# Kernel optimization log

Measured on AMD Instinct MI355X. Metric: run time of the kernel, lower is better.

The kernel has to match this reference:

```python
import jax, jax.numpy as jnp
import numpy as np

EPS = 1e-10

def _quantize_one(x, codebook):
    # x: [B, T, D]; codebook: [K, D]
    B, T, D = x.shape
    K = codebook.shape[0]
    flat = x.reshape(-1, D)  # [N, D]
    # squared euclidean distance (argmin of this == argmax of -dist in torch code)
    dist = (jnp.sum(flat * flat, axis=-1, keepdims=True)
            - 2.0 * flat @ codebook.T
            + jnp.sum(codebook * codebook, axis=-1))  # [N, K]
    ind = jnp.argmin(dist, axis=-1)  # [N]
    q = codebook[ind].reshape(B, T, D)
    # commitment loss: mse(quantize.detach(), x) * commitment(=1.0)
    loss = jnp.mean((jax.lax.stop_gradient(q) - x) ** 2)
    # straight-through estimator
    q_st = x + jax.lax.stop_gradient(q - x)
    # perplexity from one-hot encodings
    counts = jnp.zeros((K,), dtype=x.dtype).at[ind].add(1.0)
    avg_probs = counts / ind.shape[0]
    perplexity = jnp.exp(-jnp.sum(avg_probs * jnp.log(avg_probs + EPS)))
    return q_st, loss, perplexity

def setup_inputs() -> dict:
    key = jax.random.key(0)
    k1, k2 = jax.random.split(key)
    z = jax.random.normal(k1, (16, 64, 4096), dtype=jnp.float32)
    codebooks = jax.random.normal(k2, (8, 1024, 64), dtype=jnp.float32)
    return {"z": z, "codebooks": codebooks}

def reference(z, codebooks):
    # z: [B, code_dim, T] -> transpose(2,1) -> [B, T, code_dim]
    x = jnp.transpose(z, (0, 2, 1))

    def step(carry, cb):
        residual, quantized_out = carry
        q, loss, perp = _quantize_one(residual, cb)
        return (residual - q, quantized_out + q), (loss, perp)

    (_, quantized_out), (losses, perplexities) = jax.lax.scan(
        step, (x, jnp.zeros_like(x)), codebooks)
    zq = jnp.transpose(quantized_out, (0, 2, 1))  # back to [B, code_dim, T]
    return zq, losses, perplexities
```

## Files before the change

### kernel.cpp

```cpp
#include <hip/hip_runtime.h>

#define S      8
#define K      1024
#define D      64
#define NVEC   65536
#define NW     4096
#define NELEM  4194304.0f
#define EPSQ   1e-10f
#define DELTA  0.005f

typedef __attribute__((ext_vector_type(8))) short  short8;
typedef __attribute__((ext_vector_type(4))) float  float4v;

static __device__ inline unsigned short f2bf(float f) {
    unsigned int u = __float_as_uint(f);
    u = (u + 0x7FFFu + ((u >> 16) & 1u)) >> 16;
    return (unsigned short)u;
}
static __device__ inline float bf2f(unsigned short h) {
    return __uint_as_float(((unsigned int)h) << 16);
}

__global__ void rvq_prep(const float* __restrict__ cb,
                         unsigned short* __restrict__ cbi,
                         float* __restrict__ c2, unsigned* __restrict__ cnt) {
    int i = blockIdx.x * blockDim.x + threadIdx.x;
    if (i < S * K) {
        const float* row = cb + (size_t)i * D;
        float a0 = 0.f, a1 = 0.f, a2 = 0.f, a3 = 0.f;
#pragma unroll
        for (int d = 0; d < D; d += 4) {
            a0 = fmaf(row[d+0], row[d+0], a0);
            a1 = fmaf(row[d+1], row[d+1], a1);
            a2 = fmaf(row[d+2], row[d+2], a2);
            a3 = fmaf(row[d+3], row[d+3], a3);
        }
        c2[i] = (a0 + a1) + (a2 + a3);
        cnt[i] = 0u;
    }
    int s  = i >> 12;
    int tau = (i >> 6) & 63;
    int l  = i & 63;
    int m  = l & 15, qq = l >> 4;
    const float* row = cb + (size_t)(s * K + tau * 16 + m) * D;
    short8 h0h, h0l, h1h, h1l;
#pragma unroll
    for (int e = 0; e < 8; ++e) {
        float x = -2.0f * row[qq * 8 + e];
        unsigned short h = f2bf(x);
        h0h[e] = (short)h; h0l[e] = (short)f2bf(x - bf2f(h));
        float y = -2.0f * row[32 + qq * 8 + e];
        unsigned short g = f2bf(y);
        h1h[e] = (short)g; h1l[e] = (short)f2bf(y - bf2f(g));
    }
    unsigned short* rec = cbi + (size_t)(s * 64 + tau) * 2048 + l * 8;
    *(short8*)(rec +    0) = h0h;
    *(short8*)(rec +  512) = h1h;
    *(short8*)(rec + 1024) = h0l;
    *(short8*)(rec + 1536) = h1l;
}

__global__ __launch_bounds__(64, 2)
void rvq_main(const float* __restrict__ z, const float* __restrict__ cbf,
              const unsigned short* __restrict__ cbi,
              const float* __restrict__ c2, float* __restrict__ zq,
              float* __restrict__ lossp, unsigned* __restrict__ cnt) {
    const int lane = threadIdx.x;
    const int m    = lane & 15;
    const int q    = lane >> 4;
    const int wid  = blockIdx.x;
    const int vbase = wid * 16;
    const int b    = vbase >> 12;
    const int ta   = (vbase & 4095) + m;
    const size_t zrow = ((size_t)(b * 64)) << 12;
    const int lo16 = lane * 16;
    const int lom  = m * 4;

    float ra0[8], ra1[8];
#pragma unroll
    for (int i = 0; i < 8; ++i) {
        ra0[i] = z[zrow + ((size_t)(q*8+i)    << 12) + ta];
        ra1[i] = z[zrow + ((size_t)(32+q*8+i) << 12) + ta];
    }

#define LOADB(i) {                                                           \
        B##i##0 = *(const short8*)(tp + lo16);                               \
        B##i##1 = *(const short8*)(tp + lo16 + 1024);                        \
        B##i##2 = *(const short8*)(tp + lo16 + 2048);                        \
        B##i##3 = *(const short8*)(tp + lo16 + 3072);                        \
        cc##i   = *(const float*)(cp + lom);                                 \
        tp += 4096; cp += 64;                                                \
    }

#define COMPUTE(i, tt) {                                                     \
        float4v a0 = {cc##i, cc##i, cc##i, cc##i};                           \
        __builtin_amdgcn_s_setprio(1);                                       \
        a0 = __builtin_amdgcn_mfma_f32_16x16x32_bf16(xa0h, B##i##0, a0, 0,0,0); \
        a0 = __builtin_amdgcn_mfma_f32_16x16x32_bf16(xa0l, B##i##0, a0, 0,0,0); \
        a0 = __builtin_amdgcn_mfma_f32_16x16x32_bf16(xa0h, B##i##2, a0, 0,0,0); \
        a0 = __builtin_amdgcn_mfma_f32_16x16x32_bf16(xa1h, B##i##1, a0, 0,0,0); \
        a0 = __builtin_amdgcn_mfma_f32_16x16x32_bf16(xa1l, B##i##1, a0, 0,0,0); \
        a0 = __builtin_amdgcn_mfma_f32_16x16x32_bf16(xa1h, B##i##3, a0, 0,0,0); \
        __builtin_amdgcn_s_setprio(0);                                       \
        const int ncol = (tt) * 16 + m;                                      \
        _Pragma("unroll")                                                    \
        for (int j = 0; j < 4; ++j) {                                        \
            float sa = a0[j];                                                \
            b2a[j] = __builtin_amdgcn_fmed3f(sa, b1a[j], b2a[j]);            \
            k1a[j] = (sa < b1a[j]) ? ncol : k1a[j];                          \
            b1a[j] = fminf(sa, b1a[j]);                                      \
        }                                                                    \
    }

#pragma unroll 1
    for (int s = 0; s < S; ++s) {
        short8 xa0h, xa0l, xa1h, xa1l;
#pragma unroll
        for (int i = 0; i < 8; ++i) {
            unsigned short h;
            h = f2bf(ra0[i]); xa0h[i] = (short)h; xa0l[i] = (short)f2bf(ra0[i] - bf2f(h));
            h = f2bf(ra1[i]); xa1h[i] = (short)h; xa1l[i] = (short)f2bf(ra1[i] - bf2f(h));
        }

        float b1a[4], b2a[4];
        int   k1a[4];
#pragma unroll
        for (int j = 0; j < 4; ++j) {
            b1a[j] = 3.4e38f; b2a[j] = 3.4e38f; k1a[j] = 0;
        }

        const float* c2s = c2 + s * K;
        const char*  tp  = (const char*)(cbi + (size_t)s * 131072);
        const char*  cp  = (const char*)c2s;

        short8 B00, B01, B02, B03, B10, B11, B12, B13;
        float  cc0, cc1;

        LOADB(0) LOADB(1)

#pragma unroll 1
        for (int it = 0; it < 31; ++it) {
            const int tau = it * 2;
            COMPUTE(0, tau + 0) LOADB(0)
            COMPUTE(1, tau + 1) LOADB(1)
        }
        COMPUTE(0, 62) COMPUTE(1, 63)

#pragma unroll
        for (int off = 1; off < 16; off <<= 1) {
#pragma unroll
            for (int j = 0; j < 4; ++j) {
                float o1 = __shfl_xor(b1a[j], off); int ok = __shfl_xor(k1a[j], off);
                float o2 = __shfl_xor(b2a[j], off);
                float n2 = fminf(fminf(b2a[j], o2), fmaxf(b1a[j], o1));
                bool tk = (o1 < b1a[j]) || (o1 == b1a[j] && ok < k1a[j]);
                k1a[j] = tk ? ok : k1a[j]; b1a[j] = fminf(b1a[j], o1); b2a[j] = n2;
            }
        }

        const float* cr0 = cbf + (size_t)s * 65536;
#define RESCUE(b1X, b2X, k1X, R0, R1)                                         \
        for (int j = 0; j < 4; ++j) {                                         \
            unsigned long long mask = __ballot(b2X[j] - b1X[j] < DELTA);      \
            while (mask) {                                                    \
                int lq = (int)(__builtin_ctzll(mask)) >> 4;                   \
                mask &= ~(0xFFFFULL << (lq * 16));                            \
                int mrow = lq * 4 + j;                                        \
                float bd = 3.4e38f; int bk = 0;                               \
                for (int cc = 0; cc < 16; ++cc) {                             \
                    int n = cc * 64 + lane;                                   \
                    const float* crow = cr0 + (size_t)n * 64;                 \
                    float dot = 0.f;                                          \
                    for (int p2 = 0; p2 < 4; ++p2) {                          \
                        for (int i = 0; i < 8; ++i)                           \
                            dot = fmaf(__shfl(R0[i], mrow + 16*p2), crow[p2*8+i], dot); \
                        for (int i = 0; i < 8; ++i)                           \
                            dot = fmaf(__shfl(R1[i], mrow + 16*p2), crow[32+p2*8+i], dot); \
                    }                                                         \
                    float sc = c2s[n] - 2.f * dot;                            \
                    if (sc < bd) { bd = sc; bk = n; }                         \
                }                                                             \
                for (int off = 1; off < 64; off <<= 1) {                      \
                    float ob = __shfl_xor(bd, off); int ok = __shfl_xor(bk, off); \
                    bool tk = (ob < bd) || (ob == bd && ok < bk);             \
                    bk = tk ? ok : bk; bd = fminf(bd, ob);                    \
                }                                                             \
                if (q == lq) k1X[j] = bk;                                     \
            }                                                                 \
        }
        RESCUE(b1a, b2a, k1a, ra0, ra1)
#undef RESCUE

        int mm = m & 3, src = (m >> 2) * 16;
        int wa0 = __shfl(k1a[0], src), wa1 = __shfl(k1a[1], src);
        int wa2 = __shfl(k1a[2], src), wa3 = __shfl(k1a[3], src);
        int bka = (mm == 0) ? wa0 : (mm == 1) ? wa1 : (mm == 2) ? wa2 : wa3;

        const float* qa = cbf + (size_t)s * 65536 + (size_t)bka * 64;
#pragma unroll
        for (int i = 0; i < 8; ++i) {
            ra0[i] -= qa[q*8+i];  ra1[i] -= qa[32+q*8+i];
        }

        float ls = 0.f;
#pragma unroll
        for (int i = 0; i < 8; ++i) {
            ls = fmaf(ra0[i], ra0[i], ls); ls = fmaf(ra1[i], ra1[i], ls);
        }
#pragma unroll
        for (int off = 1; off < 64; off <<= 1) ls += __shfl_xor(ls, off);
        if (lane == 0) lossp[s * NW + wid] = ls;

        if (q == 0) atomicAdd(&cnt[s * K + bka], 1u);
    }
#undef LOADB
#undef COMPUTE

#pragma unroll
    for (int i = 0; i < 8; ++i) {
        size_t a0 = zrow + ((size_t)(q*8+i)    << 12) + ta;
        size_t a1 = zrow + ((size_t)(32+q*8+i) << 12) + ta;
        zq[a0] = z[a0] - ra0[i];
        zq[a1] = z[a1] - ra1[i];
    }
}

__global__ void rvq_finalize(const float* __restrict__ lossp,
                             const unsigned* __restrict__ cnt,
                             float* __restrict__ out_loss,
                             float* __restrict__ out_perp) {
    const int s   = blockIdx.x;
    const int tid = threadIdx.x;
    float ent = 0.f, lsum = 0.f;
    for (int i = tid; i < K; i += 256) {
        float p = (float)cnt[s * K + i] * (1.0f / 65536.0f);
        ent += p * logf(p + EPSQ);
    }
    for (int i = tid; i < NW; i += 256) lsum += lossp[s * NW + i];
    __shared__ float redE[4], redL[4];
#pragma unroll
    for (int off = 32; off > 0; off >>= 1) {
        ent  += __shfl_down(ent, off);
        lsum += __shfl_down(lsum, off);
    }
    if ((tid & 63) == 0) { redE[tid >> 6] = ent; redL[tid >> 6] = lsum; }
    __syncthreads();
    if (tid == 0) {
        float te = redE[0] + redE[1] + redE[2] + redE[3];
        float tl = redL[0] + redL[1] + redL[2] + redL[3];
        out_perp[s] = expf(-te);
        out_loss[s] = tl * (1.0f / NELEM);
    }
}

extern "C" void kernel_launch(void* const* d_in, const int* in_sizes, int n_in,
                              void* d_out, int out_size, void* d_ws, size_t ws_size,
                              hipStream_t stream) {
    const float* z  = (const float*)d_in[0];
    const float* cb = (const float*)d_in[1];

    float* zq       = (float*)d_out;
    float* out_loss = zq + 4194304;
    float* out_perp = out_loss + 8;

    char* ws = (char*)d_ws;
    unsigned short* cbi = (unsigned short*)(ws);
    float*    c2    = (float*)(ws + 2097152);
    unsigned* cnt   = (unsigned*)(ws + 2129920);
    float*    lossp = (float*)(ws + 2162688);

    hipLaunchKernelGGL(rvq_prep,     dim3(128),  dim3(256), 0, stream, cb, cbi, c2, cnt);
    hipLaunchKernelGGL(rvq_main,     dim3(NW),   dim3(64),  0, stream, z, cb, cbi, c2, zq, lossp, cnt);
    hipLaunchKernelGGL(rvq_finalize, dim3(S),    dim3(256), 0, stream, lossp, cnt, out_loss, out_perp);
}
```

Before: 429.1 us.

## Process 32 vectors per wave sharing codebook tiles, residuals kept in LDS

Each wave now handles two 16-vector tiles, so every codebook B-fragment loaded from memory feeds two sets of MFMAs and codebook traffic per vector is halved. The MFMA chain is split into two independent accumulators per tile to shorten dependency chains and expose more instruction-level parallelism. Residuals move from registers into a padded shared-memory array, which adds LDS traffic and lowers register pressure. The grid is halved (NW 2048), which reduces the number of waves available to hide latency.

```diff
diff --git a/kernel.cpp b/kernel.cpp
--- a/kernel.cpp
+++ b/kernel.cpp
@@ -4,7 +4,7 @@
 #define K      1024
 #define D      64
 #define NVEC   65536
-#define NW     4096
+#define NW     2048
 #define NELEM  4194304.0f
 #define EPSQ   1e-10f
 #define DELTA  0.005f
@@ -69,18 +69,22 @@
     const int m    = lane & 15;
     const int q    = lane >> 4;
     const int wid  = blockIdx.x;
-    const int vbase = wid * 16;
+    const int vbase = wid * 32;
     const int b    = vbase >> 12;
     const int ta   = (vbase & 4095) + m;
+    const int tb   = ta + 16;
     const size_t zrow = ((size_t)(b * 64)) << 12;
     const int lo16 = lane * 16;
     const int lom  = m * 4;
 
-    float ra0[8], ra1[8];
+    __shared__ float rsp[32][65];
+
 #pragma unroll
     for (int i = 0; i < 8; ++i) {
-        ra0[i] = z[zrow + ((size_t)(q*8+i)    << 12) + ta];
-        ra1[i] = z[zrow + ((size_t)(32+q*8+i) << 12) + ta];
+        rsp[m][q*8+i]         = z[zrow + ((size_t)(q*8+i)    << 12) + ta];
+        rsp[m][32+q*8+i]      = z[zrow + ((size_t)(32+q*8+i) << 12) + ta];
+        rsp[16+m][q*8+i]      = z[zrow + ((size_t)(q*8+i)    << 12) + tb];
+        rsp[16+m][32+q*8+i]   = z[zrow + ((size_t)(32+q*8+i) << 12) + tb];
     }
 
 #define LOADB(i) {                                                           \
@@ -92,41 +96,53 @@
         tp += 4096; cp += 64;                                                \
     }
 
+#define MF(A,B,C) __builtin_amdgcn_mfma_f32_16x16x32_bf16(A,B,C,0,0,0)
+
 #define COMPUTE(i, tt) {                                                     \
-        float4v a0 = {cc##i, cc##i, cc##i, cc##i};                           \
+        float4v p0 = {cc##i, cc##i, cc##i, cc##i};                           \
+        float4v p1 = {0.f, 0.f, 0.f, 0.f};                                   \
+        float4v r0 = {cc##i, cc##i, cc##i, cc##i};                           \
+        float4v r1 = {0.f, 0.f, 0.f, 0.f};                                   \
         __builtin_amdgcn_s_setprio(1);                                       \
-        a0 = __builtin_amdgcn_mfma_f32_16x16x32_bf16(xa0h, B##i##0, a0, 0,0,0); \
-        a0 = __builtin_amdgcn_mfma_f32_16x16x32_bf16(xa0l, B##i##0, a0, 0,0,0); \
-        a0 = __builtin_amdgcn_mfma_f32_16x16x32_bf16(xa0h, B##i##2, a0, 0,0,0); \
-        a0 = __builtin_amdgcn_mfma_f32_16x16x32_bf16(xa1h, B##i##1, a0, 0,0,0); \
-        a0 = __builtin_amdgcn_mfma_f32_16x16x32_bf16(xa1l, B##i##1, a0, 0,0,0); \
-        a0 = __builtin_amdgcn_mfma_f32_16x16x32_bf16(xa1h, B##i##3, a0, 0,0,0); \
+        p0 = MF(xa0h, B##i##0, p0); r0 = MF(xb0h, B##i##0, r0);              \
+        p1 = MF(xa1h, B##i##1, p1); r1 = MF(xb1h, B##i##1, r1);              \
+        p0 = MF(xa0l, B##i##0, p0); r0 = MF(xb0l, B##i##0, r0);              \
+        p1 = MF(xa1l, B##i##1, p1); r1 = MF(xb1l, B##i##1, r1);              \
+        p0 = MF(xa0h, B##i##2, p0); r0 = MF(xb0h, B##i##2, r0);              \
+        p1 = MF(xa1h, B##i##3, p1); r1 = MF(xb1h, B##i##3, r1);              \
         __builtin_amdgcn_s_setprio(0);                                       \
         const int ncol = (tt) * 16 + m;                                      \
         _Pragma("unroll")                                                    \
         for (int j = 0; j < 4; ++j) {                                        \
-            float sa = a0[j];                                                \
+            float sa = p0[j] + p1[j];                                        \
             b2a[j] = __builtin_amdgcn_fmed3f(sa, b1a[j], b2a[j]);            \
             k1a[j] = (sa < b1a[j]) ? ncol : k1a[j];                          \
             b1a[j] = fminf(sa, b1a[j]);                                      \
+            float sb = r0[j] + r1[j];                                        \
+            b2b[j] = __builtin_amdgcn_fmed3f(sb, b1b[j], b2b[j]);            \
+            k1b[j] = (sb < b1b[j]) ? ncol : k1b[j];                          \
+            b1b[j] = fminf(sb, b1b[j]);                                      \
         }                                                                    \
     }
 
 #pragma unroll 1
     for (int s = 0; s < S; ++s) {
-        short8 xa0h, xa0l, xa1h, xa1l;
+        short8 xa0h, xa0l, xa1h, xa1l, xb0h, xb0l, xb1h, xb1l;
 #pragma unroll
         for (int i = 0; i < 8; ++i) {
-            unsigned short h;
-            h = f2bf(ra0[i]); xa0h[i] = (short)h; xa0l[i] = (short)f2bf(ra0[i] - bf2f(h));
-            h = f2bf(ra1[i]); xa1h[i] = (short)h; xa1l[i] = (short)f2bf(ra1[i] - bf2f(h));
-        }
-
-        float b1a[4], b2a[4];
-        int   k1a[4];
+            unsigned short h; float v;
+            v = rsp[m][q*8+i];        h = f2bf(v); xa0h[i] = (short)h; xa0l[i] = (short)f2bf(v - bf2f(h));
+            v = rsp[m][32+q*8+i];     h = f2bf(v); xa1h[i] = (short)h; xa1l[i] = (short)f2bf(v - bf2f(h));
+            v = rsp[16+m][q*8+i];     h = f2bf(v); xb0h[i] = (short)h; xb0l[i] = (short)f2bf(v - bf2f(h));
+            v = rsp[16+m][32+q*8+i];  h = f2bf(v); xb1h[i] = (short)h; xb1l[i] = (short)f2bf(v - bf2f(h));
+        }
+
+        float b1a[4], b2a[4], b1b[4], b2b[4];
+        int   k1a[4], k1b[4];
 #pragma unroll
         for (int j = 0; j < 4; ++j) {
             b1a[j] = 3.4e38f; b2a[j] = 3.4e38f; k1a[j] = 0;
+            b1b[j] = 3.4e38f; b2b[j] = 3.4e38f; k1b[j] = 0;
         }
 
         const float* c2s = c2 + s * K;
@@ -155,11 +171,16 @@
                 float n2 = fminf(fminf(b2a[j], o2), fmaxf(b1a[j], o1));
                 bool tk = (o1 < b1a[j]) || (o1 == b1a[j] && ok < k1a[j]);
                 k1a[j] = tk ? ok : k1a[j]; b1a[j] = fminf(b1a[j], o1); b2a[j] = n2;
+                o1 = __shfl_xor(b1b[j], off); ok = __shfl_xor(k1b[j], off);
+                o2 = __shfl_xor(b2b[j], off);
+                n2 = fminf(fminf(b2b[j], o2), fmaxf(b1b[j], o1));
+                tk = (o1 < b1b[j]) || (o1 == b1b[j] && ok < k1b[j]);
+                k1b[j] = tk ? ok : k1b[j]; b1b[j] = fminf(b1b[j], o1); b2b[j] = n2;
             }
         }
 
         const float* cr0 = cbf + (size_t)s * 65536;
-#define RESCUE(b1X, b2X, k1X, R0, R1)                                         \
+#define RESCUE(b1X, b2X, k1X, ROW)                                            \
         for (int j = 0; j < 4; ++j) {                                         \
             unsigned long long mask = __ballot(b2X[j] - b1X[j] < DELTA);      \
             while (mask) {                                                    \
@@ -171,12 +192,8 @@
                     int n = cc * 64 + lane;                                   \
                     const float* crow = cr0 + (size_t)n * 64;                 \
                     float dot = 0.f;                                          \
-                    for (int p2 = 0; p2 < 4; ++p2) {                          \
-                        for (int i = 0; i < 8; ++i)                           \
-                            dot = fmaf(__shfl(R0[i], mrow + 16*p2), crow[p2*8+i], dot); \
-                        for (int i = 0; i < 8; ++i)                           \
-                            dot = fmaf(__shfl(R1[i], mrow + 16*p2), crow[32+p2*8+i], dot); \
-                    }                                                         \
+                    for (int d = 0; d < 64; ++d)                              \
+                        dot = fmaf(rsp[(ROW) + mrow][d], crow[d], dot);       \
                     float sc = c2s[n] - 2.f * dot;                            \
                     if (sc < bd) { bd = sc; bk = n; }                         \
                 }                                                             \
@@ -188,40 +205,55 @@
                 if (q == lq) k1X[j] = bk;                                     \
             }                                                                 \
         }
-        RESCUE(b1a, b2a, k1a, ra0, ra1)
+        RESCUE(b1a, b2a, k1a, 0)
+        RESCUE(b1b, b2b, k1b, 16)
 #undef RESCUE
 
         int mm = m & 3, src = (m >> 2) * 16;
         int wa0 = __shfl(k1a[0], src), wa1 = __shfl(k1a[1], src);
         int wa2 = __shfl(k1a[2], src), wa3 = __shfl(k1a[3], src);
         int bka = (mm == 0) ? wa0 : (mm == 1) ? wa1 : (mm == 2) ? wa2 : wa3;
+        int wb0 = __shfl(k1b[0], src), wb1 = __shfl(k1b[1], src);
+        int wb2 = __shfl(k1b[2], src), wb3 = __shfl(k1b[3], src);
+        int bkb = (mm == 0) ? wb0 : (mm == 1) ? wb1 : (mm == 2) ? wb2 : wb3;
 
         const float* qa = cbf + (size_t)s * 65536 + (size_t)bka * 64;
+        const float* qb = cbf + (size_t)s * 65536 + (size_t)bkb * 64;
+        float ls = 0.f;
 #pragma unroll
         for (int i = 0; i < 8; ++i) {
-            ra0[i] -= qa[q*8+i];  ra1[i] -= qa[32+q*8+i];
-        }
-
-        float ls = 0.f;
-#pragma unroll
-        for (int i = 0; i < 8; ++i) {
-            ls = fmaf(ra0[i], ra0[i], ls); ls = fmaf(ra1[i], ra1[i], ls);
+            float na = rsp[m][q*8+i]        - qa[q*8+i];
+            float nb = rsp[m][32+q*8+i]     - qa[32+q*8+i];
+            float nc = rsp[16+m][q*8+i]     - qb[q*8+i];
+            float nd = rsp[16+m][32+q*8+i]  - qb[32+q*8+i];
+            rsp[m][q*8+i] = na;        rsp[m][32+q*8+i] = nb;
+            rsp[16+m][q*8+i] = nc;     rsp[16+m][32+q*8+i] = nd;
+            ls = fmaf(na, na, ls); ls = fmaf(nb, nb, ls);
+            ls = fmaf(nc, nc, ls); ls = fmaf(nd, nd, ls);
         }
 #pragma unroll
         for (int off = 1; off < 64; off <<= 1) ls += __shfl_xor(ls, off);
         if (lane == 0) lossp[s * NW + wid] = ls;
 
-        if (q == 0) atomicAdd(&cnt[s * K + bka], 1u);
+        if (q == 0) {
+            atomicAdd(&cnt[s * K + bka], 1u);
+            atomicAdd(&cnt[s * K + bkb], 1u);
+        }
     }
 #undef LOADB
 #undef COMPUTE
+#undef MF
 
 #pragma unroll
     for (int i = 0; i < 8; ++i) {
         size_t a0 = zrow + ((size_t)(q*8+i)    << 12) + ta;
         size_t a1 = zrow + ((size_t)(32+q*8+i) << 12) + ta;
-        zq[a0] = z[a0] - ra0[i];
-        zq[a1] = z[a1] - ra1[i];
+        zq[a0] = z[a0] - rsp[m][q*8+i];
+        zq[a1] = z[a1] - rsp[m][32+q*8+i];
+        size_t a2 = zrow + ((size_t)(q*8+i)    << 12) + tb;
+        size_t a3 = zrow + ((size_t)(32+q*8+i) << 12) + tb;
+        zq[a2] = z[a2] - rsp[16+m][q*8+i];
+        zq[a3] = z[a3] - rsp[16+m][32+q*8+i];
     }
 }
 
```

Result: faster. 373.3 us (median of 3 runs) (-13.0%).

## Process 64 vectors per wave to reuse codebook fragments across four MFMA tiles

Applied to the files above, without the earlier changes.

Each wave now handles four 16-vector tiles instead of one. Every loaded codebook B fragment therefore feeds four sets of MFMAs, which cuts global/L2 codebook traffic per vector by a factor of four. The residuals move from registers into a padded shared-memory array, and the MFMA chains are split into two independent accumulators per tile so more independent work can interleave. In exchange the grid shrinks to 1024 waves, occupancy drops to one wave per SIMD, and register pressure rises from the 16 bf16 operand vectors plus four sets of argmin state.

```diff
diff --git a/kernel.cpp b/kernel.cpp
--- a/kernel.cpp
+++ b/kernel.cpp
@@ -4,7 +4,7 @@
 #define K      1024
 #define D      64
 #define NVEC   65536
-#define NW     4096
+#define NW     1024
 #define NELEM  4194304.0f
 #define EPSQ   1e-10f
 #define DELTA  0.005f
@@ -60,7 +60,7 @@
     *(short8*)(rec + 1536) = h1l;
 }
 
-__global__ __launch_bounds__(64, 2)
+__global__ __launch_bounds__(64, 1)
 void rvq_main(const float* __restrict__ z, const float* __restrict__ cbf,
               const unsigned short* __restrict__ cbi,
               const float* __restrict__ c2, float* __restrict__ zq,
@@ -69,18 +69,28 @@
     const int m    = lane & 15;
     const int q    = lane >> 4;
     const int wid  = blockIdx.x;
-    const int vbase = wid * 16;
+    const int vbase = wid * 64;
     const int b    = vbase >> 12;
     const int ta   = (vbase & 4095) + m;
+    const int tb   = ta + 16;
+    const int tc   = ta + 32;
+    const int td   = ta + 48;
     const size_t zrow = ((size_t)(b * 64)) << 12;
     const int lo16 = lane * 16;
     const int lom  = m * 4;
 
-    float ra0[8], ra1[8];
+    __shared__ float rsp[64][65];
+
 #pragma unroll
     for (int i = 0; i < 8; ++i) {
-        ra0[i] = z[zrow + ((size_t)(q*8+i)    << 12) + ta];
-        ra1[i] = z[zrow + ((size_t)(32+q*8+i) << 12) + ta];
+        rsp[m][q*8+i]       = z[zrow + ((size_t)(q*8+i)    << 12) + ta];
+        rsp[m][32+q*8+i]    = z[zrow + ((size_t)(32+q*8+i) << 12) + ta];
+        rsp[16+m][q*8+i]    = z[zrow + ((size_t)(q*8+i)    << 12) + tb];
+        rsp[16+m][32+q*8+i] = z[zrow + ((size_t)(32+q*8+i) << 12) + tb];
+        rsp[32+m][q*8+i]    = z[zrow + ((size_t)(q*8+i)    << 12) + tc];
+        rsp[32+m][32+q*8+i] = z[zrow + ((size_t)(32+q*8+i) << 12) + tc];
+        rsp[48+m][q*8+i]    = z[zrow + ((size_t)(q*8+i)    << 12) + td];
+        rsp[48+m][32+q*8+i] = z[zrow + ((size_t)(32+q*8+i) << 12) + td];
     }
 
 #define LOADB(i) {                                                           \
@@ -92,41 +102,73 @@
         tp += 4096; cp += 64;                                                \
     }
 
+#define MF(A,B,C) __builtin_amdgcn_mfma_f32_16x16x32_bf16(A,B,C,0,0,0)
+
+#define SCUP(p0, p1, b1X, b2X, k1X) {                                        \
+        _Pragma("unroll")                                                    \
+        for (int j = 0; j < 4; ++j) {                                        \
+            float sx = p0[j] + p1[j];                                        \
+            b2X[j] = __builtin_amdgcn_fmed3f(sx, b1X[j], b2X[j]);            \
+            k1X[j] = (sx < b1X[j]) ? ncol : k1X[j];                          \
+            b1X[j] = fminf(sx, b1X[j]);                                      \
+        }                                                                    \
+    }
+
 #define COMPUTE(i, tt) {                                                     \
-        float4v a0 = {cc##i, cc##i, cc##i, cc##i};                           \
+        float4v pa0 = {cc##i, cc##i, cc##i, cc##i}, pa1 = {0.f,0.f,0.f,0.f}; \
+        float4v pb0 = {cc##i, cc##i, cc##i, cc##i}, pb1 = {0.f,0.f,0.f,0.f}; \
+        float4v pc0 = {cc##i, cc##i, cc##i, cc##i}, pc1 = {0.f,0.f,0.f,0.f}; \
+        float4v pd0 = {cc##i, cc##i, cc##i, cc##i}, pd1 = {0.f,0.f,0.f,0.f}; \
         __builtin_amdgcn_s_setprio(1);                                       \
-        a0 = __builtin_amdgcn_mfma_f32_16x16x32_bf16(xa0h, B##i##0, a0, 0,0,0); \
-        a0 = __builtin_amdgcn_mfma_f32_16x16x32_bf16(xa0l, B##i##0, a0, 0,0,0); \
-        a0 = __builtin_amdgcn_mfma_f32_16x16x32_bf16(xa0h, B##i##2, a0, 0,0,0); \
-        a0 = __builtin_amdgcn_mfma_f32_16x16x32_bf16(xa1h, B##i##1, a0, 0,0,0); \
-        a0 = __builtin_amdgcn_mfma_f32_16x16x32_bf16(xa1l, B##i##1, a0, 0,0,0); \
-        a0 = __builtin_amdgcn_mfma_f32_16x16x32_bf16(xa1h, B##i##3, a0, 0,0,0); \
+        pa0 = MF(xa0h, B##i##0, pa0); pb0 = MF(xb0h, B##i##0, pb0);          \
+        pc0 = MF(xc0h, B##i##0, pc0); pd0 = MF(xd0h, B##i##0, pd0);          \
+        pa1 = MF(xa1h, B##i##1, pa1); pb1 = MF(xb1h, B##i##1, pb1);          \
+        pc1 = MF(xc1h, B##i##1, pc1); pd1 = MF(xd1h, B##i##1, pd1);          \
+        pa0 = MF(xa0l, B##i##0, pa0); pb0 = MF(xb0l, B##i##0, pb0);          \
+        pc0 = MF(xc0l, B##i##0, pc0); pd0 = MF(xd0l, B##i##0, pd0);          \
+        pa1 = MF(xa1l, B##i##1, pa1); pb1 = MF(xb1l, B##i##1, pb1);          \
+        pc1 = MF(xc1l, B##i##1, pc1); pd1 = MF(xd1l, B##i##1, pd1);          \
+        pa0 = MF(xa0h, B##i##2, pa0); pb0 = MF(xb0h, B##i##2, pb0);          \
+        pc0 = MF(xc0h, B##i##2, pc0); pd0 = MF(xd0h, B##i##2, pd0);          \
+        pa1 = MF(xa1h, B##i##3, pa1); pb1 = MF(xb1h, B##i##3, pb1);          \
+        pc1 = MF(xc1h, B##i##3, pc1); pd1 = MF(xd1h, B##i##3, pd1);          \
         __builtin_amdgcn_s_setprio(0);                                       \
         const int ncol = (tt) * 16 + m;                                      \
+        SCUP(pa0, pa1, b1a, b2a, k1a)                                        \
+        SCUP(pb0, pb1, b1b, b2b, k1b)                                        \
+        SCUP(pc0, pc1, b1c, b2c, k1c)                                        \
+        SCUP(pd0, pd1, b1d, b2d, k1d)                                        \
+    }
+
+#define REBUILD(row, xh0, xl0, xh1, xl1) {                                   \
         _Pragma("unroll")                                                    \
-        for (int j = 0; j < 4; ++j) {                                        \
-            float sa = a0[j];                                                \
-            b2a[j] = __builtin_amdgcn_fmed3f(sa, b1a[j], b2a[j]);            \
-            k1a[j] = (sa < b1a[j]) ? ncol : k1a[j];                          \
-            b1a[j] = fminf(sa, b1a[j]);                                      \
+        for (int i = 0; i < 8; ++i) {                                        \
+            unsigned short h; float v;                                       \
+            v = rsp[row][q*8+i];    h = f2bf(v);                             \
+            xh0[i] = (short)h; xl0[i] = (short)f2bf(v - bf2f(h));            \
+            v = rsp[row][32+q*8+i]; h = f2bf(v);                             \
+            xh1[i] = (short)h; xl1[i] = (short)f2bf(v - bf2f(h));            \
         }                                                                    \
     }
 
 #pragma unroll 1
     for (int s = 0; s < S; ++s) {
-        short8 xa0h, xa0l, xa1h, xa1l;
-#pragma unroll
-        for (int i = 0; i < 8; ++i) {
-            unsigned short h;
-            h = f2bf(ra0[i]); xa0h[i] = (short)h; xa0l[i] = (short)f2bf(ra0[i] - bf2f(h));
-            h = f2bf(ra1[i]); xa1h[i] = (short)h; xa1l[i] = (short)f2bf(ra1[i] - bf2f(h));
-        }
-
-        float b1a[4], b2a[4];
-        int   k1a[4];
+        short8 xa0h, xa0l, xa1h, xa1l, xb0h, xb0l, xb1h, xb1l;
+        short8 xc0h, xc0l, xc1h, xc1l, xd0h, xd0l, xd1h, xd1l;
+        REBUILD(m,      xa0h, xa0l, xa1h, xa1l)
+        REBUILD(16 + m, xb0h, xb0l, xb1h, xb1l)
+        REBUILD(32 + m, xc0h, xc0l, xc1h, xc1l)
+        REBUILD(48 + m, xd0h, xd0l, xd1h, xd1l)
+
+        float b1a[4], b2a[4], b1b[4], b2b[4];
+        float b1c[4], b2c[4], b1d[4], b2d[4];
+        int   k1a[4], k1b[4], k1c[4], k1d[4];
 #pragma unroll
         for (int j = 0; j < 4; ++j) {
             b1a[j] = 3.4e38f; b2a[j] = 3.4e38f; k1a[j] = 0;
+            b1b[j] = 3.4e38f; b2b[j] = 3.4e38f; k1b[j] = 0;
+            b1c[j] = 3.4e38f; b2c[j] = 3.4e38f; k1c[j] = 0;
+            b1d[j] = 3.4e38f; b2d[j] = 3.4e38f; k1d[j] = 0;
         }
 
         const float* c2s = c2 + s * K;
@@ -146,20 +188,27 @@
         }
         COMPUTE(0, 62) COMPUTE(1, 63)
 
-#pragma unroll
-        for (int off = 1; off < 16; off <<= 1) {
-#pragma unroll
-            for (int j = 0; j < 4; ++j) {
-                float o1 = __shfl_xor(b1a[j], off); int ok = __shfl_xor(k1a[j], off);
-                float o2 = __shfl_xor(b2a[j], off);
-                float n2 = fminf(fminf(b2a[j], o2), fmaxf(b1a[j], o1));
-                bool tk = (o1 < b1a[j]) || (o1 == b1a[j] && ok < k1a[j]);
-                k1a[j] = tk ? ok : k1a[j]; b1a[j] = fminf(b1a[j], o1); b2a[j] = n2;
-            }
-        }
+#define RED(b1X, b2X, k1X) {                                                 \
+        _Pragma("unroll")                                                    \
+        for (int off = 1; off < 16; off <<= 1) {                             \
+            _Pragma("unroll")                                                \
+            for (int j = 0; j < 4; ++j) {                                    \
+                float o1 = __shfl_xor(b1X[j], off);                          \
+                int   ok = __shfl_xor(k1X[j], off);                          \
+                float o2 = __shfl_xor(b2X[j], off);                          \
+                float n2 = fminf(fminf(b2X[j], o2), fmaxf(b1X[j], o1));      \
+                bool tk = (o1 < b1X[j]) || (o1 == b1X[j] && ok < k1X[j]);    \
+                k1X[j] = tk ? ok : k1X[j];                                   \
+                b1X[j] = fminf(b1X[j], o1); b2X[j] = n2;                     \
+            }                                                                \
+        }                                                                    \
+    }
+        RED(b1a, b2a, k1a) RED(b1b, b2b, k1b)
+        RED(b1c, b2c, k1c) RED(b1d, b2d, k1d)
+#undef RED
 
         const float* cr0 = cbf + (size_t)s * 65536;
-#define RESCUE(b1X, b2X, k1X, R0, R1)                                         \
+#define RESCUE(b1X, b2X, k1X, ROW)                                            \
         for (int j = 0; j < 4; ++j) {                                         \
             unsigned long long mask = __ballot(b2X[j] - b1X[j] < DELTA);      \
             while (mask) {                                                    \
@@ -171,12 +220,8 @@
                     int n = cc * 64 + lane;                                   \
                     const float* crow = cr0 + (size_t)n * 64;                 \
                     float dot = 0.f;                                          \
-                    for (int p2 = 0; p2 < 4; ++p2) {                          \
-                        for (int i = 0; i < 8; ++i)                           \
-                            dot = fmaf(__shfl(R0[i], mrow + 16*p2), crow[p2*8+i], dot); \
-                        for (int i = 0; i < 8; ++i)                           \
-                            dot = fmaf(__shfl(R1[i], mrow + 16*p2), crow[32+p2*8+i], dot); \
-                    }                                                         \
+                    for (int d = 0; d < 64; ++d)                              \
+                        dot = fmaf(rsp[(ROW) + mrow][d], crow[d], dot);       \
                     float sc = c2s[n] - 2.f * dot;                            \
                     if (sc < bd) { bd = sc; bk = n; }                         \
                 }                                                             \
@@ -188,40 +233,54 @@
                 if (q == lq) k1X[j] = bk;                                     \
             }                                                                 \
         }
-        RESCUE(b1a, b2a, k1a, ra0, ra1)
+        RESCUE(b1a, b2a, k1a, 0)
+        RESCUE(b1b, b2b, k1b, 16)
+        RESCUE(b1c, b2c, k1c, 32)
+        RESCUE(b1d, b2d, k1d, 48)
 #undef RESCUE
 
         int mm = m & 3, src = (m >> 2) * 16;
-        int wa0 = __shfl(k1a[0], src), wa1 = __shfl(k1a[1], src);
-        int wa2 = __shfl(k1a[2], src), wa3 = __shfl(k1a[3], src);
-        int bka = (mm == 0) ? wa0 : (mm == 1) ? wa1 : (mm == 2) ? wa2 : wa3;
-
-        const float* qa = cbf + (size_t)s * 65536 + (size_t)bka * 64;
-#pragma unroll
-        for (int i = 0; i < 8; ++i) {
-            ra0[i] -= qa[q*8+i];  ra1[i] -= qa[32+q*8+i];
-        }
-
         float ls = 0.f;
-#pragma unroll
-        for (int i = 0; i < 8; ++i) {
-            ls = fmaf(ra0[i], ra0[i], ls); ls = fmaf(ra1[i], ra1[i], ls);
-        }
+#define FINISH(k1X, ROW) {                                                   \
+        int w0 = __shfl(k1X[0], src), w1 = __shfl(k1X[1], src);              \
+        int w2 = __shfl(k1X[2], src), w3 = __shfl(k1X[3], src);              \
+        int bk = (mm == 0) ? w0 : (mm == 1) ? w1 : (mm == 2) ? w2 : w3;      \
+        const float* qv = cbf + (size_t)s * 65536 + (size_t)bk * 64;         \
+        _Pragma("unroll")                                                    \
+        for (int i = 0; i < 8; ++i) {                                        \
+            float n0 = rsp[(ROW)+m][q*8+i]    - qv[q*8+i];                   \
+            float n1 = rsp[(ROW)+m][32+q*8+i] - qv[32+q*8+i];                \
+            rsp[(ROW)+m][q*8+i] = n0;  rsp[(ROW)+m][32+q*8+i] = n1;          \
+            ls = fmaf(n0, n0, ls); ls = fmaf(n1, n1, ls);                    \
+        }                                                                    \
+        if (q == 0) atomicAdd(&cnt[s * K + bk], 1u);                         \
+    }
+        FINISH(k1a, 0)
+        FINISH(k1b, 16)
+        FINISH(k1c, 32)
+        FINISH(k1d, 48)
+#undef FINISH
 #pragma unroll
         for (int off = 1; off < 64; off <<= 1) ls += __shfl_xor(ls, off);
         if (lane == 0) lossp[s * NW + wid] = ls;
-
-        if (q == 0) atomicAdd(&cnt[s * K + bka], 1u);
     }
 #undef LOADB
 #undef COMPUTE
+#undef SCUP
+#undef REBUILD
 
 #pragma unroll
     for (int i = 0; i < 8; ++i) {
-        size_t a0 = zrow + ((size_t)(q*8+i)    << 12) + ta;
-        size_t a1 = zrow + ((size_t)(32+q*8+i) << 12) + ta;
-        zq[a0] = z[a0] - ra0[i];
-        zq[a1] = z[a1] - ra1[i];
+        size_t a0 = zrow + ((size_t)(q*8+i)    << 12);
+        size_t a1 = zrow + ((size_t)(32+q*8+i) << 12);
+        zq[a0 + ta] = z[a0 + ta] - rsp[m][q*8+i];
+        zq[a1 + ta] = z[a1 + ta] - rsp[m][32+q*8+i];
+        zq[a0 + tb] = z[a0 + tb] - rsp[16+m][q*8+i];
+        zq[a1 + tb] = z[a1 + tb] - rsp[16+m][32+q*8+i];
+        zq[a0 + tc] = z[a0 + tc] - rsp[32+m][q*8+i];
+        zq[a1 + tc] = z[a1 + tc] - rsp[32+m][32+q*8+i];
+        zq[a0 + td] = z[a0 + td] - rsp[48+m][q*8+i];
+        zq[a1 + td] = z[a1 + td] - rsp[48+m][32+q*8+i];
     }
 }
 
```

New measurement: 465.4 us. +8.5%, slower.
